# Kernel tuning notes

Hardware: AMD Instinct MI355X
Metric: run time of the kernel (lower is better)

Reference implementation:

```python
import jax, jax.numpy as jnp
import numpy as np

B, C, H, W = 1, 512, 64, 64
HEADS, DH = 8, 64
DI = HEADS * DH          # 512 = heads * dim_head
SW = 8                   # sliding window size
CB = 16                  # compress block size
SB = 2                   # selection block size
NSEL = 2                 # num selected blocks
N = H * W                # 4096 tokens
NCB = N // CB            # 256 compress blocks
NFB = N // SB            # 2048 fine (selection) blocks
NEG = jnp.finfo(jnp.float32).min


def setup_inputs() -> dict:
    key = jax.random.key(0)
    ks = jax.random.split(key, 24)
    rn = lambda k, shape, s=0.03: jax.random.normal(k, shape, jnp.float32) * s
    return dict(
        x=jax.random.normal(ks[0], (B, C, H, W), jnp.float32),
        w_in=rn(ks[1], (C, C)), b_in=jnp.zeros((C,), jnp.float32),
        g_norm=jnp.ones((C,), jnp.float32),
        wq=rn(ks[2], (DI, C)), wk=rn(ks[3], (DI, C)), wv=rn(ks[4], (DI, C)),
        k_pos=rn(ks[5], (HEADS, CB, DH), 0.02), v_pos=rn(ks[6], (HEADS, CB, DH), 0.02),
        mem_k=rn(ks[7], (HEADS, 1, DH), 0.02), mem_v=rn(ks[8], (HEADS, 1, DH), 0.02),
        kc_w1=rn(ks[9], (CB * DH, CB * DH)), kc_b1=jnp.zeros((CB * DH,), jnp.float32),
        kc_w2=rn(ks[10], (DH, CB * DH)), kc_b2=jnp.zeros((DH,), jnp.float32),
        vc_w1=rn(ks[11], (CB * DH, CB * DH)), vc_b1=jnp.zeros((CB * DH,), jnp.float32),
        vc_w2=rn(ks[12], (DH, CB * DH)), vc_b2=jnp.zeros((DH,), jnp.float32),
        w_strat=rn(ks[13], (3 * HEADS, C)), b_strat=jnp.zeros((3 * HEADS,), jnp.float32),
        w_comb=rn(ks[14], (C, DI)),
        w_out=rn(ks[15], (C, C)), b_out=jnp.zeros((C,), jnp.float32),
    )


def _rope(x):
    # rotary-embedding-torch default: theta=10000, interleaved pairs
    d = x.shape[-1]
    inv = 1.0 / (10000.0 ** (jnp.arange(0, d, 2, dtype=jnp.float32) / d))
    ang = jnp.arange(x.shape[-2], dtype=jnp.float32)[:, None] * inv  # (n, d/2)
    cos = jnp.repeat(jnp.cos(ang), 2, axis=-1)
    sin = jnp.repeat(jnp.sin(ang), 2, axis=-1)
    xp = x.reshape(x.shape[:-1] + (d // 2, 2))
    xr = jnp.stack((-xp[..., 1], xp[..., 0]), axis=-1).reshape(x.shape)
    return x * cos + xr * sin


def reference(x, w_in, b_in, g_norm, wq, wk, wv, k_pos, v_pos, mem_k, mem_v,
              kc_w1, kc_b1, kc_w2, kc_b2, vc_w1, vc_b1, vc_w2, vc_b2,
              w_strat, b_strat, w_comb, w_out, b_out):
    scale = DH ** -0.5
    # proj_in (1x1 conv) then flatten to sequence (b, n, c); residual uses this
    xs = jnp.einsum('bchw,oc->bohw', x, w_in) + b_in[None, :, None, None]
    seq = xs.reshape(B, C, N).transpose(0, 2, 1)
    # RMSNorm
    h = seq * jax.lax.rsqrt(jnp.mean(seq * seq, -1, keepdims=True) + 1e-6) * g_norm
    # qkv -> (b, heads, n, d)
    q = (h @ wq.T).reshape(B, N, HEADS, DH).transpose(0, 2, 1, 3)
    k = (h @ wk.T).reshape(B, N, HEADS, DH).transpose(0, 2, 1, 3)
    v = (h @ wv.T).reshape(B, N, HEADS, DH).transpose(0, 2, 1, 3)

    # ---- 1. compressed attention (block compression MLP + mem kv) ----
    kin = (k + jnp.tile(k_pos, (1, NCB, 1))[None]).reshape(B, HEADS, NCB, CB * DH)
    vin = (v + jnp.tile(v_pos, (1, NCB, 1))[None]).reshape(B, HEADS, NCB, CB * DH)
    ck = jax.nn.relu(kin @ kc_w1.T + kc_b1) @ kc_w2.T + kc_b2   # (b,h,NCB,d)
    cv = jax.nn.relu(vin @ vc_w1.T + vc_b1) @ vc_w2.T + vc_b2
    ck = jnp.concatenate([jnp.broadcast_to(mem_k[None], (B, HEADS, 1, DH)), ck], axis=2)
    cv = jnp.concatenate([jnp.broadcast_to(mem_v[None], (B, HEADS, 1, DH)), cv], axis=2)
    ck_seq = jnp.concatenate([jnp.array([-1]), (jnp.arange(NCB) + 1) * CB - 1])
    cmask = ck_seq[None, :] < jnp.arange(N)[:, None]             # (N, NCB+1), True=attend
    csim = jnp.einsum('bhid,bhjd->bhij', q, ck) * scale
    csim = jnp.where(cmask[None, None], csim, NEG)
    compressed_out = jnp.einsum('bhij,bhjd->bhid', jax.nn.softmax(csim, axis=-1), cv)

    # rotary positions for fine + sliding branches
    rq, rk = _rope(q), _rope(k)

    # ---- 2. fine selection attention ----
    # importance at fine-block granularity; since SB divides CB, each fine block
    # maps to exactly one compress block (equivalent to repeat->mask->mean in torch)
    imp = csim[..., 1:]                                          # drop mem kv logits
    fb_of = jnp.arange(NFB) // (CB // SB)
    imp_fine = imp[..., fb_of]                                   # (b,h,N,NFB)
    blk_causal = jnp.arange(NFB)[None, :] < (jnp.arange(N) // SB)[:, None]
    imp_fine = jnp.where(blk_causal[None, None], imp_fine, -jnp.inf)
    logits = jnp.concatenate([jnp.full((B, HEADS, N, 1), -1e3, jnp.float32), imp_fine], axis=-1)
    probs = jax.nn.softmax(logits, axis=-1)[..., 1:]             # (b,h,N,NFB)
    sel_val, sel_idx = jax.lax.top_k(probs, NSEL)                # (b,h,N,NSEL)
    diag_idx = jnp.broadcast_to((jnp.arange(N) // SB)[None, None, :, None], (B, HEADS, N, 1))
    sel_idx = jnp.concatenate([sel_idx, diag_idx], axis=-1)      # append own (diagonal) block
    fmask_sel = jnp.repeat((sel_val > 1e-10)[..., None], SB, axis=-1)   # (b,h,N,NSEL,SB)
    diag_mask = jnp.arange(SB)[None, :] <= (jnp.arange(N) % SB)[:, None]  # within-block causal
    diag_mask = jnp.broadcast_to(diag_mask[None, None, :, None, :], (B, HEADS, N, 1, SB))
    fmask = jnp.concatenate([fmask_sel, diag_mask], axis=-2).reshape(B, HEADS, N, (NSEL + 1) * SB)
    fk_blk = rk.reshape(B, HEADS, NFB, SB, DH)
    fv_blk = v.reshape(B, HEADS, NFB, SB, DH)
    idx = sel_idx.reshape(B, HEADS, N * (NSEL + 1))[..., None, None]
    fk = jnp.take_along_axis(fk_blk, idx, axis=2).reshape(B, HEADS, N, (NSEL + 1) * SB, DH)
    fv = jnp.take_along_axis(fv_blk, idx, axis=2).reshape(B, HEADS, N, (NSEL + 1) * SB, DH)
    fsim = jnp.einsum('bhid,bhijd->bhij', rq, fk) * scale
    fsim = jnp.where(fmask, fsim, NEG)
    fine_out = jnp.einsum('bhij,bhijd->bhid', jax.nn.softmax(fsim, axis=-1), fv)

    # ---- 3. sliding window attention (causal, exact window: 0 <= i-j <= SW) ----
    kp = jnp.pad(rk, ((0, 0), (0, 0), (SW, 0), (0, 0)))
    vp = jnp.pad(v, ((0, 0), (0, 0), (SW, 0), (0, 0)))
    widx = jnp.arange(N)[:, None] + jnp.arange(SW + 1)[None, :]  # indices into padded seq
    kw = kp[:, :, widx]                                          # (b,h,N,SW+1,d)
    vw = vp[:, :, widx]
    wvalid = (jnp.arange(N)[:, None] - SW + jnp.arange(SW + 1)[None, :]) >= 0
    ssim = jnp.einsum('bhid,bhijd->bhij', rq, kw) * scale
    ssim = jnp.where(wvalid[None, None], ssim, NEG)
    slide_out = jnp.einsum('bhij,bhijd->bhid', jax.nn.softmax(ssim, axis=-1), vw)

    # ---- combine the three strategies with learned sigmoid gates ----
    gates = jax.nn.sigmoid(h @ w_strat.T + b_strat).reshape(B, N, HEADS, 3).transpose(0, 2, 1, 3)
    out = gates[..., 0:1] * compressed_out + gates[..., 1:2] * fine_out + gates[..., 2:3] * slide_out
    out = out.transpose(0, 2, 1, 3).reshape(B, N, DI) @ w_comb.T  # merge heads + combine
    out2d = out.transpose(0, 2, 1).reshape(B, C, H, W)
    return jnp.einsum('bchw,oc->bohw', out2d, w_out) + b_out[None, :, None, None] + xs
```

## Files before the change

### kernel.cpp

```cpp
#include <hip/hip_runtime.h>
#include <hip/hip_bf16.h>
#include <math.h>

typedef __attribute__((ext_vector_type(8))) short s8v;
typedef __attribute__((ext_vector_type(8))) _Float16 h8v;
typedef __attribute__((ext_vector_type(4))) float f4v;
typedef __hip_bfloat16 bf16;

#define NEGF (-3.40282346638528859812e+38f)
#define QSMEM 20480

enum { EPI_F32 = 0, EPI_BIAS, EPI_BRELU_BF16, EPI_BF16, EPI_FINAL };

__device__ __forceinline__ float wred_sum(float v) {
#pragma unroll
  for (int m = 1; m < 64; m <<= 1) v += __shfl_xor(v, m, 64);
  return v;
}

template <int EPI>
__device__ __forceinline__ void bgemm_body(char* smem, int bx, int by, int bz,
    const bf16* __restrict__ A, const bf16* __restrict__ B, void* __restrict__ C,
    int K, int ldC, long sA, long sB, long sC,
    const float* __restrict__ bias, const void* __restrict__ aux) {
  short (*Ahs)[2048] = (short(*)[2048])smem;
  short (*Bhs)[2048] = (short(*)[2048])(smem + 2 * 2048 * 2);
  const short* ah = (const short*)A + (long)bz * sA;
  const short* bh = (const short*)B + (long)bz * sB;
  int tid = threadIdx.x;
  int wv_ = tid >> 6, lane = tid & 63;
  int lrow = tid >> 2, lcol = (tid & 3) << 3;
  int lidx = lrow * 32 + lcol;
  long abase = (long)(bx * 64 + lrow) * K + lcol;
  long bbase = (long)(by * 64 + lrow) * K + lcol;
  int frow = lane & 15, fk = (lane >> 4) << 3;
  int aoff = (wv_ * 16 + frow) * 32 + fk;
  f4v acc[4] = {};
  {
    s8v avh = *(const s8v*)&ah[abase];
    s8v bvh = *(const s8v*)&bh[bbase];
    *(s8v*)&Ahs[0][lidx] = avh;
    *(s8v*)&Bhs[0][lidx] = bvh;
  }
  __syncthreads();
  int nit = K >> 5, buf = 0;
  for (int it = 0; it < nit; it++) {
    s8v avh, bvh;
    bool pf = (it + 1 < nit);
    if (pf) {
      long ko = (long)(it + 1) << 5;
      avh = *(const s8v*)&ah[abase + ko];
      bvh = *(const s8v*)&bh[bbase + ko];
    }
    s8v afh = *(const s8v*)&Ahs[buf][aoff];
#pragma unroll
    for (int nt = 0; nt < 4; nt++) {
      s8v bfh = *(const s8v*)&Bhs[buf][(nt * 16 + frow) * 32 + fk];
      acc[nt] = __builtin_amdgcn_mfma_f32_16x16x32_bf16(afh, bfh, acc[nt], 0, 0, 0);
    }
    if (pf) {
      *(s8v*)&Ahs[buf ^ 1][lidx] = avh;
      *(s8v*)&Bhs[buf ^ 1][lidx] = bvh;
      __syncthreads();
      buf ^= 1;
    }
  }
  int rb = bx * 64 + wv_ * 16 + ((lane >> 4) << 2);
#pragma unroll
  for (int nt = 0; nt < 4; nt++) {
    int gn = by * 64 + nt * 16 + (lane & 15);
#pragma unroll
    for (int rg = 0; rg < 4; rg++) {
      int gm = rb + rg;
      float v = acc[nt][rg];
      long ci = (long)bz * sC + (long)gm * ldC + gn;
      if (EPI == EPI_F32) ((float*)C)[ci] = v;
      else if (EPI == EPI_BIAS) ((float*)C)[ci] = v + bias[gn];
      else if (EPI == EPI_BRELU_BF16) ((bf16*)C)[ci] = __float2bfloat16(fmaxf(v + bias[gn], 0.f));
      else if (EPI == EPI_BF16) ((bf16*)C)[ci] = __float2bfloat16(v);
      else if (EPI == EPI_FINAL)
        ((float*)C)[ci] = v + bias[gm] + ((const float*)aux)[(long)gn * 512 + gm];
    }
  }
}


#define HX_DECL                                                     \
  short* L = (short*)smem;                                          \
  const int MS = 64 * 40;                                           \
  int tid = threadIdx.x;                                            \
  int wv = tid >> 6, lane = tid & 63;                               \
  int lrow = tid >> 2, lcol = (tid & 3) << 3;                       \
  int frow = lane & 15, fk = (lane >> 4) << 3;                      \
  int aoff = (wv * 16 + frow) * 40 + fk;                            \
  int soff = lrow * 40 + lcol;                                      \
  f4v acc0[4] = {}, accx[4] = {}, acc2[4] = {};

#define HX_STAGE0                                                   \
  {                                                                 \
    *(h8v*)&L[0 * MS + soff] = *(const h8v*)&Ah[abase];             \
    *(h8v*)&L[1 * MS + soff] = *(const h8v*)&Al[abase];             \
    *(h8v*)&L[2 * MS + soff] = *(const h8v*)&Bh[bbase];             \
    *(h8v*)&L[3 * MS + soff] = *(const h8v*)&Bl[bbase];             \
  }                                                                 \
  __syncthreads();

#define HX_LOOP(NIT)                                                \
  for (int it = 0; it < (NIT); it++) {                              \
    h8v pah, pal, pbh, pbl;                                         \
    bool pf = (it + 1 < (NIT));                                     \
    if (pf) {                                                       \
      long ko = (long)(it + 1) << 5;                                \
      pah = *(const h8v*)&Ah[abase + ko];                           \
      pal = *(const h8v*)&Al[abase + ko];                           \
      pbh = *(const h8v*)&Bh[bbase + ko];                           \
      pbl = *(const h8v*)&Bl[bbase + ko];                           \
    }                                                               \
    h8v ah = *(const h8v*)&L[aoff];                                 \
    h8v al = *(const h8v*)&L[MS + aoff];                            \
    _Pragma("unroll") for (int nt = 0; nt < 4; nt++) {              \
      int bo = 2 * MS + (nt * 16 + frow) * 40 + fk;                 \
      h8v bh = *(const h8v*)&L[bo];                                 \
      h8v bl = *(const h8v*)&L[bo + MS];                            \
      acc0[nt] = __builtin_amdgcn_mfma_f32_16x16x32_f16(ah, bh, acc0[nt], 0, 0, 0); \
      accx[nt] = __builtin_amdgcn_mfma_f32_16x16x32_f16(ah, bl, accx[nt], 0, 0, 0); \
      accx[nt] = __builtin_amdgcn_mfma_f32_16x16x32_f16(al, bh, accx[nt], 0, 0, 0); \
      acc2[nt] = __builtin_amdgcn_mfma_f32_16x16x32_f16(al, bl, acc2[nt], 0, 0, 0); \
    }                                                               \
    if (pf) {                                                       \
      __syncthreads();                                              \
      *(h8v*)&L[soff] = pah;                                        \
      *(h8v*)&L[MS + soff] = pal;                                   \
      *(h8v*)&L[2 * MS + soff] = pbh;                               \
      *(h8v*)&L[3 * MS + soff] = pbl;                               \
      __syncthreads();                                              \
    }                                                               \
  }

#define HX_COMBINE(nt, rg) \
  (acc0[nt][rg] + (accx[nt][rg] + acc2[nt][rg] * (1.f / 4096.f)) * (1.f / 4096.f))

__device__ __forceinline__ void qk_f16_body(char* smem, int bx, int by,
    const _Float16* __restrict__ Ah, const _Float16* __restrict__ Al,
    const _Float16* __restrict__ Bh, const _Float16* __restrict__ Bl,
    _Float16* __restrict__ qhh, _Float16* __restrict__ qhl,
    _Float16* __restrict__ kinh, _Float16* __restrict__ kinl,
    float* __restrict__ rq, float* __restrict__ rk, const float* __restrict__ kpos) {
  HX_DECL
  long abase = (long)(bx * 64 + lrow) * 512 + lcol;
  long bbase = (long)(by * 64 + lrow) * 512 + lcol;
  HX_STAGE0
  HX_LOOP(16)
  bool isq = by < 8;
  int h = by & 7;
  int rb = wv * 16 + ((lane >> 4) << 2);
#pragma unroll
  for (int nt = 0; nt < 4; nt++) {
    int dloc = nt * 16 + frow;
    int d2 = dloc >> 1;
    float inv = exp2f((float)d2 * -0.4152410118609203f);
#pragma unroll
    for (int rg = 0; rg < 4; rg++) {
      int n = bx * 64 + rb + rg;
      float vf = HX_COMBINE(nt, rg);
      float ang = (float)n * inv;
      float sv, cv;
      sincosf(ang, &sv, &cv);
      float vp = __shfl_xor(vf, 1, 64);
      float rr = (dloc & 1) ? (vf * cv + vp * sv) : (vf * cv - vp * sv);
      long oi = ((long)h * 4096 + n) * 64 + dloc;
      if (isq) {
        _Float16 hi = (_Float16)vf;
        qhh[oi] = hi;
        qhl[oi] = (_Float16)((vf - (float)hi) * 4096.f);
        rq[oi] = rr;
      } else {
        rk[oi] = rr;
        float kv = vf + kpos[(h * 16 + (n & 15)) * 64 + dloc];
        _Float16 khi = (_Float16)kv;
        long ki = (((long)h * 256 + (n >> 4)) * 16 + (n & 15)) * 64 + dloc;
        kinh[ki] = khi;
        kinl[ki] = (_Float16)((kv - (float)khi) * 4096.f);
      }
    }
  }
}

__device__ __forceinline__ void hx_conv_body(char* smem, int bx, int by,
    const _Float16* __restrict__ Ah, const _Float16* __restrict__ Al,
    const _Float16* __restrict__ Bh, const _Float16* __restrict__ Bl,
    float* __restrict__ C, const float* __restrict__ bias) {
  HX_DECL
  long abase = (long)(bx * 64 + lrow) * 512 + lcol;
  long bbase = (long)(by * 64 + lrow) * 512 + lcol;
  HX_STAGE0
  HX_LOOP(16)
  int rb = bx * 64 + wv * 16 + ((lane >> 4) << 2);
#pragma unroll
  for (int nt = 0; nt < 4; nt++) {
    int gn = by * 64 + nt * 16 + frow;
#pragma unroll
    for (int rg = 0; rg < 4; rg++) {
      int gm = rb + rg;
      C[(long)gm * 512 + gn] = HX_COMBINE(nt, rg) + bias[gn];
    }
  }
}

__device__ __forceinline__ void hx_mlp1_body(char* smem, int bx, int by,
    const _Float16* __restrict__ Ah, const _Float16* __restrict__ Al,
    const _Float16* __restrict__ Bh, const _Float16* __restrict__ Bl,
    _Float16* __restrict__ Ch, _Float16* __restrict__ Cl, const float* __restrict__ bias) {
  HX_DECL
  long abase = (long)(bx * 64 + lrow) * 1024 + lcol;
  long bbase = (long)(by * 64 + lrow) * 1024 + lcol;
  HX_STAGE0
  HX_LOOP(32)
  int rb = bx * 64 + wv * 16 + ((lane >> 4) << 2);
#pragma unroll
  for (int nt = 0; nt < 4; nt++) {
    int gn = by * 64 + nt * 16 + frow;
#pragma unroll
    for (int rg = 0; rg < 4; rg++) {
      int gm = rb + rg;
      float v = fmaxf(HX_COMBINE(nt, rg) + bias[gn], 0.f);
      _Float16 hi = (_Float16)v;
      long ci = (long)gm * 1024 + gn;
      Ch[ci] = hi;
      Cl[ci] = (_Float16)((v - (float)hi) * 4096.f);
    }
  }
}

__device__ __forceinline__ void hx_ksplit_body(char* smem, int bx, int by,
    const _Float16* __restrict__ Ah, const _Float16* __restrict__ Al,
    const _Float16* __restrict__ Bh, const _Float16* __restrict__ Bl,
    float* __restrict__ P) {
  HX_DECL
  long kbeg = (long)by << 7;
  long abase = (long)(bx * 64 + lrow) * 1024 + kbeg + lcol;
  long bbase = (long)lrow * 1024 + kbeg + lcol;
  HX_STAGE0
  HX_LOOP(4)
  float* p = P + (long)by * 131072;
  int rb = bx * 64 + wv * 16 + ((lane >> 4) << 2);
#pragma unroll
  for (int nt = 0; nt < 4; nt++) {
    int gn = nt * 16 + frow;
#pragma unroll
    for (int rg = 0; rg < 4; rg++) {
      int gm = rb + rg;
      p[(long)gm * 64 + gn] = HX_COMBINE(nt, rg);
    }
  }
}

__device__ __forceinline__ void hx_csim_body(char* smem, int bx, int by, int bz,
    const _Float16* __restrict__ Ah, const _Float16* __restrict__ Al,
    const _Float16* __restrict__ Bh, const _Float16* __restrict__ Bl,
    float* __restrict__ C) {
  HX_DECL
  long abase = ((long)bz * 4096 + bx * 64 + lrow) * 64 + lcol;
  long bbase = ((long)bz * 320 + by * 64 + lrow) * 64 + lcol;
  HX_STAGE0
  HX_LOOP(2)
  int rb = bx * 64 + wv * 16 + ((lane >> 4) << 2);
#pragma unroll
  for (int nt = 0; nt < 4; nt++) {
    int gn = by * 64 + nt * 16 + frow;
#pragma unroll
    for (int rg = 0; rg < 4; rg++) {
      int gm = rb + rg;
      C[((long)bz * 4096 + gm) * 320 + gn] = HX_COMBINE(nt, rg) * 0.125f;
    }
  }
}

__device__ __forceinline__ void prep_elem(long i,
    const float* __restrict__ wq, const float* __restrict__ wk, const float* __restrict__ wv,
    const float* __restrict__ wst, const float* __restrict__ bst,
    const float* __restrict__ kc_w1, const float* __restrict__ kc_w2,
    const float* __restrict__ vc_w1, const float* __restrict__ vc_w2, const float* __restrict__ w_comb,
    const float* __restrict__ w_out, _Float16* __restrict__ wqkh, _Float16* __restrict__ wqkl,
    bf16* __restrict__ wvs, float* __restrict__ bias2,
    _Float16* __restrict__ kw1h, _Float16* __restrict__ kw1l,
    _Float16* __restrict__ kw2h, _Float16* __restrict__ kw2l, bf16* __restrict__ vw1b,
    bf16* __restrict__ vw2b, bf16* __restrict__ wcombb, bf16* __restrict__ woutb) {
  if (i < 524288) {
    int r = (int)(i >> 9), c = (int)(i & 511);
    float w = (r < 512) ? wq[i] : wk[(r - 512) * 512 + c];
    _Float16 hi = (_Float16)w;
    wqkh[i] = hi;
    wqkl[i] = (_Float16)((w - (float)hi) * 4096.f);
    return;
  }
  i -= 524288;
  if (i < 294912) {
    int r = (int)(i >> 9), c = (int)(i & 511);
    float v = 0.f;
    if (r < 512) v = wv[i];
    else if (r < 536) v = wst[(r - 512) * 512 + c];
    wvs[i] = __float2bfloat16(v);
    if (i < 576) bias2[i] = (i >= 512 && i < 536) ? bst[i - 512] : 0.f;
    return;
  }
  i -= 294912;
  if (i < 1048576) {
    float w = kc_w1[i];
    _Float16 hi = (_Float16)w;
    kw1h[i] = hi;
    kw1l[i] = (_Float16)((w - (float)hi) * 4096.f);
    return;
  }
  i -= 1048576;
  if (i < 65536) {
    float w = kc_w2[i];
    _Float16 hi = (_Float16)w;
    kw2h[i] = hi;
    kw2l[i] = (_Float16)((w - (float)hi) * 4096.f);
    return;
  }
  i -= 65536;
  if (i < 1048576) { vw1b[i] = __float2bfloat16(vc_w1[i]); return; }
  i -= 1048576;
  if (i < 65536) { vw2b[i] = __float2bfloat16(vc_w2[i]); return; }
  i -= 65536;
  if (i < 262144) { wcombb[i] = __float2bfloat16(w_comb[i]); return; }
  i -= 262144;
  if (i < 262144) woutb[i] = __float2bfloat16(w_out[i]);
}
#define PREP_TOTAL 3571712l

template <int EPI>
__global__ __launch_bounds__(256) void gemm_bt(
    const bf16* __restrict__ A, const bf16* __restrict__ B, void* __restrict__ C,
    int K, int ldC, long sA, long sB, long sC,
    const float* __restrict__ bias, const void* __restrict__ aux) {
  __shared__ char smem[4 * 2048 * 2];
  bgemm_body<EPI>(smem, blockIdx.x, blockIdx.y, blockIdx.z, A, B, C, K, ldC, sA, sB, sC, bias, aux);
}

__global__ __launch_bounds__(256) void k_conv_prep(
    const _Float16* __restrict__ xth, const _Float16* __restrict__ xtl,
    const _Float16* __restrict__ winh, const _Float16* __restrict__ winl,
    float* __restrict__ xsf, const float* __restrict__ b_in,
    const float* __restrict__ wq, const float* __restrict__ wk, const float* __restrict__ wv,
    const float* __restrict__ wst, const float* __restrict__ bst,
    const float* __restrict__ kc_w1, const float* __restrict__ kc_w2,
    const float* __restrict__ vc_w1, const float* __restrict__ vc_w2, const float* __restrict__ w_comb,
    const float* __restrict__ w_out, _Float16* __restrict__ wqkh, _Float16* __restrict__ wqkl,
    bf16* __restrict__ wvs, float* __restrict__ bias2,
    _Float16* __restrict__ kw1h, _Float16* __restrict__ kw1l,
    _Float16* __restrict__ kw2h, _Float16* __restrict__ kw2l, bf16* __restrict__ vw1b,
    bf16* __restrict__ vw2b, bf16* __restrict__ wcombb, bf16* __restrict__ woutb) {
  __shared__ char smem[QSMEM];
  if (blockIdx.y < 8) {
    hx_conv_body(smem, blockIdx.x, blockIdx.y, xth, xtl, winh, winl, xsf, b_in);
  } else {
    long base = (((long)(blockIdx.y - 8) * 64 + blockIdx.x) * 256) + threadIdx.x;
    for (long i = base; i < PREP_TOTAL; i += 16l * 64 * 256)
      prep_elem(i, wq, wk, wv, wst, bst, kc_w1, kc_w2, vc_w1, vc_w2, w_comb, w_out,
                wqkh, wqkl, wvs, bias2, kw1h, kw1l, kw2h, kw2l, vw1b, vw2b, wcombb, woutb);
  }
}

__global__ __launch_bounds__(256) void k_fused_qk_t2(
    const _Float16* __restrict__ hhi, const _Float16* __restrict__ hlo,
    const _Float16* __restrict__ wqkh, const _Float16* __restrict__ wqkl,
    _Float16* __restrict__ qhh, _Float16* __restrict__ qhl,
    _Float16* __restrict__ kinh, _Float16* __restrict__ kinl,
    float* __restrict__ rq, float* __restrict__ rk, const float* __restrict__ kpos,
    const bf16* __restrict__ hbf, const bf16* __restrict__ wvs, float* __restrict__ T2,
    const float* __restrict__ bias2) {
  __shared__ char smem[QSMEM];
  if (blockIdx.y >= 16) {
    bgemm_body<EPI_BIAS>(smem, blockIdx.x, blockIdx.y - 16, 0, hbf, wvs, T2, 512, 576, 0, 0, 0, bias2,
                         nullptr);
    return;
  }
  qk_f16_body(smem, blockIdx.x, blockIdx.y, hhi, hlo, wqkh, wqkl, qhh, qhl, kinh, kinl, rq, rk, kpos);
}

__global__ void k_repackV(const float* __restrict__ T2, const float* __restrict__ vpos,
                          float* __restrict__ vvv, bf16* __restrict__ vin) {
  int e = blockIdx.x * 256 + threadIdx.x;
  int d = e & 63, n = (e >> 6) & 4095, h = e >> 18;
  float v0 = T2[(long)n * 576 + h * 64 + d];
  vvv[((long)h * 4096 + n) * 64 + d] = v0;
  vin[(((long)h * 256 + (n >> 4)) * 16 + (n & 15)) * 64 + d] =
      __float2bfloat16(v0 + vpos[(h * 16 + (n & 15)) * 64 + d]);
}

__global__ __launch_bounds__(256) void k_fused_mlp1(
    const _Float16* __restrict__ kinh, const _Float16* __restrict__ kinl,
    const _Float16* __restrict__ kw1h, const _Float16* __restrict__ kw1l,
    _Float16* __restrict__ hidh, _Float16* __restrict__ hidl, const float* __restrict__ kb1,
    const bf16* __restrict__ vin, const bf16* __restrict__ vw1,
    bf16* __restrict__ hidv, const float* __restrict__ vb1) {
  __shared__ char smem[QSMEM];
  if (blockIdx.y < 16)
    hx_mlp1_body(smem, blockIdx.x, blockIdx.y, kinh, kinl, kw1h, kw1l, hidh, hidl, kb1);
  else
    bgemm_body<EPI_BRELU_BF16>(smem, blockIdx.x, blockIdx.y - 16, 0, vin, vw1, hidv, 1024, 1024, 0, 0, 0,
                               vb1, nullptr);
}

__global__ __launch_bounds__(256) void k_fused_mlp2(
    const _Float16* __restrict__ hidh, const _Float16* __restrict__ hidl,
    const _Float16* __restrict__ kw2h, const _Float16* __restrict__ kw2l, float* __restrict__ kpart,
    const bf16* __restrict__ hidv, const bf16* __restrict__ vw2, float* __restrict__ cvc,
    const float* __restrict__ vb2) {
  __shared__ char smem[QSMEM];
  if (blockIdx.y < 8)
    hx_ksplit_body(smem, blockIdx.x, blockIdx.y, hidh, hidl, kw2h, kw2l, kpart);
  else
    bgemm_body<EPI_BIAS>(smem, blockIdx.x, 0, 0, hidv, vw2, cvc, 1024, 64, 0, 0, 0, vb2, nullptr);
}

__global__ __launch_bounds__(256) void k_csim(
    const _Float16* __restrict__ qhh, const _Float16* __restrict__ qhl,
    const _Float16* __restrict__ ckbh, const _Float16* __restrict__ ckbl, float* __restrict__ csim) {
  __shared__ char smem[QSMEM];
  hx_csim_body(smem, blockIdx.x, blockIdx.y, blockIdx.z, qhh, qhl, ckbh, ckbl, csim);
}

__global__ void k_transpose16(const float* __restrict__ x, _Float16* __restrict__ xth,
                              _Float16* __restrict__ xtl,
                              const float* __restrict__ w_in, _Float16* __restrict__ winh,
                              _Float16* __restrict__ winl) {
  if (blockIdx.y == 16) {
    int tid = threadIdx.y * 32 + threadIdx.x;
    long base = (long)blockIdx.x * 256 + tid;
    for (long i = base; i < 262144; i += 128l * 256) {
      float w = w_in[i];
      _Float16 hi = (_Float16)w;
      winh[i] = hi;
      winl[i] = (_Float16)((w - (float)hi) * 4096.f);
    }
    return;
  }
  __shared__ float t[32][33];
  int n0 = blockIdx.x * 32, c0 = blockIdx.y * 32;
  int tx = threadIdx.x, ty = threadIdx.y;
#pragma unroll
  for (int r = ty; r < 32; r += 8) t[r][tx] = x[(long)(c0 + r) * 4096 + n0 + tx];
  __syncthreads();
#pragma unroll
  for (int r = ty; r < 32; r += 8) {
    float v = t[tx][r];
    _Float16 hi = (_Float16)v;
    long o = (long)(n0 + r) * 512 + c0 + tx;
    xth[o] = hi;
    xtl[o] = (_Float16)((v - (float)hi) * 4096.f);
  }
}

__global__ __launch_bounds__(256) void k_rmsnorm(const float* __restrict__ xs, const float* __restrict__ g,
                                                 _Float16* __restrict__ hhi, _Float16* __restrict__ hlo,
                                                 bf16* __restrict__ hbf) {
  int n = blockIdx.x, t = threadIdx.x;
  const float* row = xs + (long)n * 512;
  double a = (double)row[t], b = (double)row[t + 256];
  double ss = a * a + b * b;
#pragma unroll
  for (int m = 1; m < 64; m <<= 1) ss += __shfl_xor(ss, m, 64);
  __shared__ double red[4];
  if ((t & 63) == 0) red[t >> 6] = ss;
  __syncthreads();
  double tot = red[0] + red[1] + red[2] + red[3];
  double r = 1.0 / sqrt(tot / 512.0 + 1e-6);
  double h0 = a * r * (double)g[t], h1 = b * r * (double)g[t + 256];
  long o = (long)n * 512 + t;
  float f0 = (float)h0, f1 = (float)h1;
  _Float16 a0 = (_Float16)f0, a1 = (_Float16)f1;
  hhi[o] = a0;
  hhi[o + 256] = a1;
  hlo[o] = (_Float16)((f0 - (float)a0) * 4096.f);
  hlo[o + 256] = (_Float16)((f1 - (float)a1) * 4096.f);
  hbf[o] = __float2bfloat16(f0);
  hbf[o + 256] = __float2bfloat16(f1);
}

__global__ void k_repackB(const float* __restrict__ kpart, const float* __restrict__ cvc,
                          const float* __restrict__ mem_k, const float* __restrict__ mem_v,
                          const float* __restrict__ kb2, _Float16* __restrict__ ckbh,
                          _Float16* __restrict__ ckbl, bf16* __restrict__ cvtb) {
  int g = blockIdx.x * 256 + threadIdx.x;
  if (g < 8 * 320 * 64) {
    int d = g & 63, j = (g >> 6) % 320, h = g / (320 * 64);
    float vf = 0.f;
    if (j == 0) vf = mem_k[h * 64 + d];
    else if (j < 257) {
      long ri = ((long)h * 256 + (j - 1)) * 64 + d;
      double s = 0.0;
#pragma unroll
      for (int p = 0; p < 8; p++) s += (double)kpart[(long)p * 131072 + ri];
      vf = (float)(s + (double)kb2[d]);
    }
    _Float16 hi = (_Float16)vf;
    ckbh[g] = hi;
    ckbl[g] = (_Float16)((vf - (float)hi) * 4096.f);
  }
  if (g < 8 * 64 * 288) {
    int j = g % 288, d = (g / 288) & 63, h = g / (288 * 64);
    float v = 0.f;
    if (j == 0) v = mem_v[h * 64 + d];
    else if (j < 257) v = cvc[((long)h * 256 + (j - 1)) * 64 + d];
    cvtb[g] = __float2bfloat16(v);
  }
}

__global__ __launch_bounds__(256) void k_selsm(const float* __restrict__ csim, bf16* __restrict__ pb,
                                               int4* __restrict__ selb) {
  int r = blockIdx.x * 4 + (threadIdx.x >> 6);
  int lane = threadIdx.x & 63;
  int i = r & 4095;
  const float* row = csim + (long)r * 320;
  int nv = i / 16 + 1;
  float s[5], e[5];
  float mx = -INFINITY;
#pragma unroll
  for (int t = 0; t < 5; t++) {
    int j = lane + 64 * t;
    float v = (j < nv) ? row[j] : -INFINITY;
    s[t] = v;
    mx = fmaxf(mx, v);
  }
#pragma unroll
  for (int m = 1; m < 64; m <<= 1) mx = fmaxf(mx, __shfl_xor(mx, m, 64));
  float sum = 0.f;
#pragma unroll
  for (int t = 0; t < 5; t++) {
    int j = lane + 64 * t;
    e[t] = (j < nv) ? __expf(s[t] - mx) : 0.f;
    sum += e[t];
  }
  sum = wred_sum(sum);
  float rinv = 1.f / sum;
  bf16* prow = pb + (long)r * 288;
#pragma unroll
  for (int t = 0; t < 5; t++) {
    int j = lane + 64 * t;
    if (j < 288) prow[j] = __float2bfloat16((j < nv) ? e[t] * rinv : 0.f);
  }
  int nvb = i >> 1;
  int nmv = (nvb + 7) >> 3;
  float vm[4];
  float bestv = -INFINITY;
  int bestm = 0x7fffffff;
#pragma unroll
  for (int t = 0; t < 4; t++) {
    int m = lane + 64 * t;
    float v = -INFINITY;
    if (m < nmv) v = (m + 1 < nv) ? row[m + 1] : NEGF;
    vm[t] = v;
    if (v > bestv) { bestv = v; bestm = m; }
  }
#pragma unroll
  for (int mk = 1; mk < 64; mk <<= 1) {
    float ov = __shfl_xor(bestv, mk, 64);
    int om = __shfl_xor(bestm, mk, 64);
    if (ov > bestv || (ov == bestv && om < bestm)) { bestv = ov; bestm = om; }
  }
  int m0 = bestm;
  int cnt0 = min(8, nvb - 8 * m0);
  float rv = -INFINITY;
  int rm = 0x7fffffff;
#pragma unroll
  for (int t = 0; t < 4; t++) {
    int m = lane + 64 * t;
    if (m != m0 && vm[t] > rv) { rv = vm[t]; rm = m; }
  }
#pragma unroll
  for (int mk = 1; mk < 64; mk <<= 1) {
    float ov = __shfl_xor(rv, mk, 64);
    int om = __shfl_xor(rm, mk, 64);
    if (ov > rv || (ov == rv && om < rm)) { rv = ov; rm = om; }
  }
  float Ml = fmaxf(-1000.f, bestv);
  float z = 0.f;
#pragma unroll
  for (int t = 0; t < 4; t++) {
    int m = lane + 64 * t;
    if (m < nmv) z += (float)min(8, nvb - 8 * m) * expf(vm[t] - Ml);
  }
  z = wred_sum(z) + expf(-1000.f - Ml);
  int fb0 = 0, fb1 = 0, mk0 = 0, mk1 = 0;
  if (nmv > 0) {
    float sv0 = expf(bestv - Ml) / z;
    fb0 = 8 * m0;
    mk0 = sv0 > 1e-10f;
    if (cnt0 >= 2) { fb1 = fb0 + 1; mk1 = mk0; }
    else if (nmv > 1) {
      float sv1 = expf(rv - Ml) / z;
      fb1 = 8 * rm;
      mk1 = sv1 > 1e-10f;
    }
  }
  if (lane == 0) selb[r] = make_int4(fb0, fb1, mk0, mk1);
}

__global__ __launch_bounds__(256) void k_fineslide(const float* __restrict__ rq, const float* __restrict__ rk,
                                                   const float* __restrict__ vv, const float* __restrict__ co,
                                                   const int4* __restrict__ selb, const float* __restrict__ T2,
                                                   bf16* __restrict__ comb) {
  int r = blockIdx.x * 4 + (threadIdx.x >> 6);
  int d = threadIdx.x & 63;
  int h = r >> 12, i = r & 4095;
  long hb = (long)h * 4096 * 64;
  float qd = rq[hb + (long)i * 64 + d];
  int4 s4 = selb[r];
  int dg = i >> 1;
  int tok[6] = {2 * s4.x, 2 * s4.x + 1, 2 * s4.y, 2 * s4.y + 1, 2 * dg, 2 * dg + 1};
  int ok6[6] = {s4.z, s4.z, s4.w, s4.w, 1, (i & 1)};
  float sim[6], val[6];
#pragma unroll
  for (int j = 0; j < 6; j++) {
    float kd = rk[hb + (long)tok[j] * 64 + d];
    val[j] = vv[hb + (long)tok[j] * 64 + d];
    float p = wred_sum(qd * kd);
    sim[j] = ok6[j] ? p * 0.125f : NEGF;
  }
  float mx = sim[0];
#pragma unroll
  for (int j = 1; j < 6; j++) mx = fmaxf(mx, sim[j]);
  float den = 0.f, fo = 0.f;
#pragma unroll
  for (int j = 0; j < 6; j++) {
    float e_ = __expf(sim[j] - mx);
    den += e_;
    fo += e_ * val[j];
  }
  fo /= den;
  float ssim[9], sval[9];
#pragma unroll
  for (int t = 0; t < 9; t++) {
    int tk = i - 8 + t;
    int okt = tk >= 0;
    int tc = okt ? tk : 0;
    float kd = rk[hb + (long)tc * 64 + d];
    sval[t] = okt ? vv[hb + (long)tc * 64 + d] : 0.f;
    float p = wred_sum(qd * kd);
    ssim[t] = okt ? p * 0.125f : NEGF;
  }
  float mx2 = ssim[8];
#pragma unroll
  for (int t = 0; t < 8; t++) mx2 = fmaxf(mx2, ssim[t]);
  float den2 = 0.f, so = 0.f;
#pragma unroll
  for (int t = 0; t < 9; t++) {
    float e_ = __expf(ssim[t] - mx2);
    den2 += e_;
    so += e_ * sval[t];
  }
  so /= den2;
  const float* gb = T2 + (long)i * 576 + 512 + h * 3;
  float g0 = 1.f / (1.f + __expf(-gb[0]));
  float g1 = 1.f / (1.f + __expf(-gb[1]));
  float g2 = 1.f / (1.f + __expf(-gb[2]));
  float cd = co[hb + (long)i * 64 + d];
  comb[(long)i * 512 + h * 64 + d] = __float2bfloat16(g0 * cd + g1 * fo + g2 * so);
}

extern "C" void kernel_launch(void* const* d_in, const int* in_sizes, int n_in, void* d_out, int out_size,
                              void* d_ws, size_t ws_size, hipStream_t stream) {
  (void)in_sizes; (void)n_in; (void)out_size; (void)ws_size;
  const float* x = (const float*)d_in[0];
  const float* w_in = (const float*)d_in[1];
  const float* b_in = (const float*)d_in[2];
  const float* g_norm = (const float*)d_in[3];
  const float* wq = (const float*)d_in[4];
  const float* wk = (const float*)d_in[5];
  const float* wv = (const float*)d_in[6];
  const float* k_pos = (const float*)d_in[7];
  const float* v_pos = (const float*)d_in[8];
  const float* mem_k = (const float*)d_in[9];
  const float* mem_v = (const float*)d_in[10];
  const float* kc_w1 = (const float*)d_in[11];
  const float* kc_b1 = (const float*)d_in[12];
  const float* kc_w2 = (const float*)d_in[13];
  const float* kc_b2 = (const float*)d_in[14];
  const float* vc_w1 = (const float*)d_in[15];
  const float* vc_b1 = (const float*)d_in[16];
  const float* vc_w2 = (const float*)d_in[17];
  const float* vc_b2 = (const float*)d_in[18];
  const float* w_strat = (const float*)d_in[19];
  const float* b_strat = (const float*)d_in[20];
  const float* w_comb = (const float*)d_in[21];
  const float* w_out = (const float*)d_in[22];
  const float* b_out = (const float*)d_in[23];

  char* wsp = (char*)d_ws;
  size_t off = 0;
  auto alloc = [&](size_t b) -> void* {
    void* p = wsp + off;
    off += (b + 255) & ~(size_t)255;
    return p;
  };
  float* xsf = (float*)alloc(4096l * 512 * 4);
  _Float16* hhi = (_Float16*)alloc(4096l * 512 * 2);
  _Float16* hlo = (_Float16*)alloc(4096l * 512 * 2);
  bf16* hbf = (bf16*)alloc(4096l * 512 * 2);
  _Float16* winh = (_Float16*)alloc(512l * 512 * 2);
  _Float16* winl = (_Float16*)alloc(512l * 512 * 2);
  _Float16* wqkh = (_Float16*)alloc(1024l * 512 * 2);
  _Float16* wqkl = (_Float16*)alloc(1024l * 512 * 2);
  bf16* wvs = (bf16*)alloc(576l * 512 * 2);
  float* bias2 = (float*)alloc(576 * 4);
  float* T2 = (float*)alloc(4096l * 576 * 4);
  float* csim = (float*)alloc(8l * 4096 * 320 * 4);
  _Float16* qhh = (_Float16*)alloc(8l * 4096 * 64 * 2);
  _Float16* qhl = (_Float16*)alloc(8l * 4096 * 64 * 2);
  float* rq = (float*)alloc(8l * 4096 * 64 * 4);
  float* rk = (float*)alloc(8l * 4096 * 64 * 4);
  float* vvb = (float*)alloc(8l * 4096 * 64 * 4);
  char* xthl = (char*)alloc(2l * 4096 * 512 * 2);
  _Float16* xth = (_Float16*)xthl;
  _Float16* xtl = xth + 4096l * 512;
  _Float16* hidh = xth;
  _Float16* hidl = xtl;
  char* kinpb = (char*)alloc(2048l * 1024 * 8 + 2048l * 1024 * 2);
  _Float16* kinh = (_Float16*)kinpb;
  _Float16* kinl = kinh + 2048l * 1024;
  bf16* vinb = (bf16*)(kinpb + 2l * 2048 * 1024 * 2);
  bf16* pb = (bf16*)kinpb;
  _Float16* kw1h = (_Float16*)alloc(1024l * 1024 * 2);
  _Float16* kw1l = (_Float16*)alloc(1024l * 1024 * 2);
  _Float16* kw2h = (_Float16*)alloc(64l * 1024 * 2);
  _Float16* kw2l = (_Float16*)alloc(64l * 1024 * 2);
  bf16* vw1b = (bf16*)alloc(1024l * 1024 * 2);
  bf16* vw2b = (bf16*)alloc(64l * 1024 * 2);
  bf16* hidv = (bf16*)alloc(2048l * 1024 * 2);
  float* cvc = (float*)alloc(2048l * 64 * 4);
  _Float16* ckbh = (_Float16*)alloc(8l * 320 * 64 * 2);
  _Float16* ckbl = (_Float16*)alloc(8l * 320 * 64 * 2);
  bf16* cvtb = (bf16*)alloc(8l * 64 * 288 * 2);
  int4* selb = (int4*)alloc(32768l * 16);
  float* co = (float*)alloc(8l * 4096 * 64 * 4);
  bf16* comb = (bf16*)alloc(4096l * 512 * 2);
  bf16* zb = (bf16*)alloc(4096l * 512 * 2);
  bf16* wcombb = (bf16*)alloc(512l * 512 * 2);
  bf16* woutb = (bf16*)alloc(512l * 512 * 2);
  float* kpart = (float*)alloc(8l * 2048 * 64 * 4);

  k_transpose16<<<dim3(128, 17), dim3(32, 8), 0, stream>>>(x, xth, xtl, w_in, winh, winl);
  k_conv_prep<<<dim3(64, 24), 256, 0, stream>>>(xth, xtl, winh, winl, xsf, b_in, wq, wk, wv, w_strat,
                                                b_strat, kc_w1, kc_w2, vc_w1, vc_w2, w_comb, w_out,
                                                wqkh, wqkl, wvs, bias2, kw1h, kw1l, kw2h, kw2l,
                                                vw1b, vw2b, wcombb, woutb);
  k_rmsnorm<<<4096, 256, 0, stream>>>(xsf, g_norm, hhi, hlo, hbf);
  k_fused_qk_t2<<<dim3(64, 25, 1), 256, 0, stream>>>(hhi, hlo, wqkh, wqkl, qhh, qhl, kinh, kinl, rq, rk,
                                                     k_pos, hbf, wvs, T2, bias2);
  k_repackV<<<8192, 256, 0, stream>>>(T2, v_pos, vvb, vinb);
  k_fused_mlp1<<<dim3(32, 32, 1), 256, 0, stream>>>(kinh, kinl, kw1h, kw1l, hidh, hidl, kc_b1, vinb, vw1b,
                                                    hidv, vc_b1);
  k_fused_mlp2<<<dim3(32, 9, 1), 256, 0, stream>>>(hidh, hidl, kw2h, kw2l, kpart, hidv, vw2b, cvc, vc_b2);
  k_repackB<<<640, 256, 0, stream>>>(kpart, cvc, mem_k, mem_v, kc_b2, ckbh, ckbl, cvtb);
  k_csim<<<dim3(64, 5, 8), 256, 0, stream>>>(qhh, qhl, ckbh, ckbl, csim);
  k_selsm<<<8192, 256, 0, stream>>>(csim, pb, selb);
  gemm_bt<EPI_F32><<<dim3(64, 1, 8), 256, 0, stream>>>(pb, cvtb, co, 288, 64, 4096l * 288, 64l * 288,
                                                       4096l * 64, nullptr, nullptr);
  k_fineslide<<<8192, 256, 0, stream>>>(rq, rk, vvb, co, selb, T2, comb);
  gemm_bt<EPI_BF16><<<dim3(64, 8, 1), 256, 0, stream>>>(comb, wcombb, zb, 512, 512, 0, 0, 0, nullptr, nullptr);
  gemm_bt<EPI_FINAL><<<dim3(8, 64, 1), 256, 0, stream>>>(woutb, zb, d_out, 512, 4096, 0, 0, 0, b_out, xsf);
}
```

Baseline: 331.5 us.

## Pad GEMM LDS, double-register prefetch, precompute rope table, skip masked csim tiles

Pads the bf16 GEMM shared-memory row stride to 40 to reduce LDS bank conflicts. Both the bf16 and split-f16 GEMM loops are unrolled by two with two register sets, so global loads for tile k+2 are issued while tile k is computed. Rope sin/cos values are computed once into a table in the transpose kernel instead of calling sincosf in the QK epilogue. The compressed-similarity kernel early-exits for tiles that are entirely causally masked, which relies on downstream code never reading those unwritten entries.

```diff
diff --git a/kernel.cpp b/kernel.cpp
--- a/kernel.cpp
+++ b/kernel.cpp
@@ -9,6 +9,7 @@
 
 #define NEGF (-3.40282346638528859812e+38f)
 #define QSMEM 20480
+#define BSMEM 20480
 
 enum { EPI_F32 = 0, EPI_BIAS, EPI_BRELU_BF16, EPI_BF16, EPI_FINAL };
 
@@ -23,18 +24,18 @@
     const bf16* __restrict__ A, const bf16* __restrict__ B, void* __restrict__ C,
     int K, int ldC, long sA, long sB, long sC,
     const float* __restrict__ bias, const void* __restrict__ aux) {
-  short (*Ahs)[2048] = (short(*)[2048])smem;
-  short (*Bhs)[2048] = (short(*)[2048])(smem + 2 * 2048 * 2);
+  short (*Ahs)[2560] = (short(*)[2560])smem;
+  short (*Bhs)[2560] = (short(*)[2560])(smem + 2 * 2560 * 2);
   const short* ah = (const short*)A + (long)bz * sA;
   const short* bh = (const short*)B + (long)bz * sB;
   int tid = threadIdx.x;
   int wv_ = tid >> 6, lane = tid & 63;
   int lrow = tid >> 2, lcol = (tid & 3) << 3;
-  int lidx = lrow * 32 + lcol;
+  int lidx = lrow * 40 + lcol;
   long abase = (long)(bx * 64 + lrow) * K + lcol;
   long bbase = (long)(by * 64 + lrow) * K + lcol;
   int frow = lane & 15, fk = (lane >> 4) << 3;
-  int aoff = (wv_ * 16 + frow) * 32 + fk;
+  int aoff = (wv_ * 16 + frow) * 40 + fk;
   f4v acc[4] = {};
   {
     s8v avh = *(const s8v*)&ah[abase];
@@ -44,27 +45,46 @@
   }
   __syncthreads();
   int nit = K >> 5, buf = 0;
-  for (int it = 0; it < nit; it++) {
-    s8v avh, bvh;
-    bool pf = (it + 1 < nit);
-    if (pf) {
-      long ko = (long)(it + 1) << 5;
-      avh = *(const s8v*)&ah[abase + ko];
-      bvh = *(const s8v*)&bh[bbase + ko];
-    }
-    s8v afh = *(const s8v*)&Ahs[buf][aoff];
-#pragma unroll
-    for (int nt = 0; nt < 4; nt++) {
-      s8v bfh = *(const s8v*)&Bhs[buf][(nt * 16 + frow) * 32 + fk];
-      acc[nt] = __builtin_amdgcn_mfma_f32_16x16x32_bf16(afh, bfh, acc[nt], 0, 0, 0);
-    }
-    if (pf) {
-      *(s8v*)&Ahs[buf ^ 1][lidx] = avh;
-      *(s8v*)&Bhs[buf ^ 1][lidx] = bvh;
+  s8v rAa, rAb, rBa, rBb;
+  if (nit > 1) {
+    rAa = *(const s8v*)&ah[abase + 32];
+    rAb = *(const s8v*)&bh[bbase + 32];
+  }
+#define B_DSMFMA                                                       \
+  {                                                                    \
+    s8v afh = *(const s8v*)&Ahs[buf][aoff];                            \
+    _Pragma("unroll") for (int nt = 0; nt < 4; nt++) {                 \
+      s8v bfh = *(const s8v*)&Bhs[buf][(nt * 16 + frow) * 40 + fk];    \
+      acc[nt] = __builtin_amdgcn_mfma_f32_16x16x32_bf16(afh, bfh, acc[nt], 0, 0, 0); \
+    }                                                                  \
+  }
+  for (int it = 0; it < nit; it += 2) {
+    if (it + 2 < nit) {
+      long ko = (long)(it + 2) << 5;
+      rBa = *(const s8v*)&ah[abase + ko];
+      rBb = *(const s8v*)&bh[bbase + ko];
+    }
+    B_DSMFMA
+    if (it + 1 < nit) {
+      *(s8v*)&Ahs[buf ^ 1][lidx] = rAa;
+      *(s8v*)&Bhs[buf ^ 1][lidx] = rAb;
       __syncthreads();
       buf ^= 1;
-    }
-  }
+      if (it + 3 < nit) {
+        long ko = (long)(it + 3) << 5;
+        rAa = *(const s8v*)&ah[abase + ko];
+        rAb = *(const s8v*)&bh[bbase + ko];
+      }
+      B_DSMFMA
+      if (it + 2 < nit) {
+        *(s8v*)&Ahs[buf ^ 1][lidx] = rBa;
+        *(s8v*)&Bhs[buf ^ 1][lidx] = rBb;
+        __syncthreads();
+        buf ^= 1;
+      }
+    }
+  }
+#undef B_DSMFMA
   int rb = bx * 64 + wv_ * 16 + ((lane >> 4) << 2);
 #pragma unroll
   for (int nt = 0; nt < 4; nt++) {
@@ -105,17 +125,8 @@
   }                                                                 \
   __syncthreads();
 
-#define HX_LOOP(NIT)                                                \
-  for (int it = 0; it < (NIT); it++) {                              \
-    h8v pah, pal, pbh, pbl;                                         \
-    bool pf = (it + 1 < (NIT));                                     \
-    if (pf) {                                                       \
-      long ko = (long)(it + 1) << 5;                                \
-      pah = *(const h8v*)&Ah[abase + ko];                           \
-      pal = *(const h8v*)&Al[abase + ko];                           \
-      pbh = *(const h8v*)&Bh[bbase + ko];                           \
-      pbl = *(const h8v*)&Bl[bbase + ko];                           \
-    }                                                               \
+#define HX_DSMFMA                                                   \
+  {                                                                 \
     h8v ah = *(const h8v*)&L[aoff];                                 \
     h8v al = *(const h8v*)&L[MS + aoff];                            \
     _Pragma("unroll") for (int nt = 0; nt < 4; nt++) {              \
@@ -127,13 +138,48 @@
       accx[nt] = __builtin_amdgcn_mfma_f32_16x16x32_f16(al, bh, accx[nt], 0, 0, 0); \
       acc2[nt] = __builtin_amdgcn_mfma_f32_16x16x32_f16(al, bl, acc2[nt], 0, 0, 0); \
     }                                                               \
-    if (pf) {                                                       \
+  }
+
+#define HX_LOOP(NIT)                                                \
+  h8v rAa, rAb, rAc, rAd, rBa, rBb, rBc, rBd;                       \
+  if ((NIT) > 1) {                                                  \
+    rAa = *(const h8v*)&Ah[abase + 32];                             \
+    rAb = *(const h8v*)&Al[abase + 32];                             \
+    rAc = *(const h8v*)&Bh[bbase + 32];                             \
+    rAd = *(const h8v*)&Bl[bbase + 32];                             \
+  }                                                                 \
+  for (int it = 0; it < (NIT); it += 2) {                           \
+    if (it + 2 < (NIT)) {                                           \
+      long ko = (long)(it + 2) << 5;                                \
+      rBa = *(const h8v*)&Ah[abase + ko];                           \
+      rBb = *(const h8v*)&Al[abase + ko];                           \
+      rBc = *(const h8v*)&Bh[bbase + ko];                           \
+      rBd = *(const h8v*)&Bl[bbase + ko];                           \
+    }                                                               \
+    HX_DSMFMA                                                       \
+    if (it + 1 < (NIT)) {                                           \
       __syncthreads();                                              \
-      *(h8v*)&L[soff] = pah;                                        \
-      *(h8v*)&L[MS + soff] = pal;                                   \
-      *(h8v*)&L[2 * MS + soff] = pbh;                               \
-      *(h8v*)&L[3 * MS + soff] = pbl;                               \
+      *(h8v*)&L[soff] = rAa;                                        \
+      *(h8v*)&L[MS + soff] = rAb;                                   \
+      *(h8v*)&L[2 * MS + soff] = rAc;                               \
+      *(h8v*)&L[3 * MS + soff] = rAd;                               \
       __syncthreads();                                              \
+      if (it + 3 < (NIT)) {                                         \
+        long ko = (long)(it + 3) << 5;                              \
+        rAa = *(const h8v*)&Ah[abase + ko];                         \
+        rAb = *(const h8v*)&Al[abase + ko];                         \
+        rAc = *(const h8v*)&Bh[bbase + ko];                         \
+        rAd = *(const h8v*)&Bl[bbase + ko];                         \
+      }                                                             \
+      HX_DSMFMA                                                     \
+      if (it + 2 < (NIT)) {                                         \
+        __syncthreads();                                            \
+        *(h8v*)&L[soff] = rBa;                                      \
+        *(h8v*)&L[MS + soff] = rBb;                                 \
+        *(h8v*)&L[2 * MS + soff] = rBc;                             \
+        *(h8v*)&L[3 * MS + soff] = rBd;                             \
+        __syncthreads();                                            \
+      }                                                             \
     }                                                               \
   }
 
@@ -145,7 +191,8 @@
     const _Float16* __restrict__ Bh, const _Float16* __restrict__ Bl,
     _Float16* __restrict__ qhh, _Float16* __restrict__ qhl,
     _Float16* __restrict__ kinh, _Float16* __restrict__ kinl,
-    float* __restrict__ rq, float* __restrict__ rk, const float* __restrict__ kpos) {
+    float* __restrict__ rq, float* __restrict__ rk, const float* __restrict__ kpos,
+    const float2* __restrict__ ropet) {
   HX_DECL
   long abase = (long)(bx * 64 + lrow) * 512 + lcol;
   long bbase = (long)(by * 64 + lrow) * 512 + lcol;
@@ -158,14 +205,12 @@
   for (int nt = 0; nt < 4; nt++) {
     int dloc = nt * 16 + frow;
     int d2 = dloc >> 1;
-    float inv = exp2f((float)d2 * -0.4152410118609203f);
 #pragma unroll
     for (int rg = 0; rg < 4; rg++) {
       int n = bx * 64 + rb + rg;
       float vf = HX_COMBINE(nt, rg);
-      float ang = (float)n * inv;
-      float sv, cv;
-      sincosf(ang, &sv, &cv);
+      float2 cs = ropet[(long)n * 32 + d2];
+      float sv = cs.x, cv = cs.y;
       float vp = __shfl_xor(vf, 1, 64);
       float rr = (dloc & 1) ? (vf * cv + vp * sv) : (vf * cv - vp * sv);
       long oi = ((long)h * 4096 + n) * 64 + dloc;
@@ -336,7 +381,7 @@
     const bf16* __restrict__ A, const bf16* __restrict__ B, void* __restrict__ C,
     int K, int ldC, long sA, long sB, long sC,
     const float* __restrict__ bias, const void* __restrict__ aux) {
-  __shared__ char smem[4 * 2048 * 2];
+  __shared__ char smem[BSMEM];
   bgemm_body<EPI>(smem, blockIdx.x, blockIdx.y, blockIdx.z, A, B, C, K, ldC, sA, sB, sC, bias, aux);
 }
 
@@ -370,6 +415,7 @@
     _Float16* __restrict__ qhh, _Float16* __restrict__ qhl,
     _Float16* __restrict__ kinh, _Float16* __restrict__ kinl,
     float* __restrict__ rq, float* __restrict__ rk, const float* __restrict__ kpos,
+    const float2* __restrict__ ropet,
     const bf16* __restrict__ hbf, const bf16* __restrict__ wvs, float* __restrict__ T2,
     const float* __restrict__ bias2) {
   __shared__ char smem[QSMEM];
@@ -378,7 +424,8 @@
                          nullptr);
     return;
   }
-  qk_f16_body(smem, blockIdx.x, blockIdx.y, hhi, hlo, wqkh, wqkl, qhh, qhl, kinh, kinl, rq, rk, kpos);
+  qk_f16_body(smem, blockIdx.x, blockIdx.y, hhi, hlo, wqkh, wqkl, qhh, qhl, kinh, kinl, rq, rk, kpos,
+              ropet);
 }
 
 __global__ void k_repackV(const float* __restrict__ T2, const float* __restrict__ vpos,
@@ -420,6 +467,7 @@
 __global__ __launch_bounds__(256) void k_csim(
     const _Float16* __restrict__ qhh, const _Float16* __restrict__ qhl,
     const _Float16* __restrict__ ckbh, const _Float16* __restrict__ ckbl, float* __restrict__ csim) {
+  if (blockIdx.y * 64 > blockIdx.x * 4 + 3) return;
   __shared__ char smem[QSMEM];
   hx_csim_body(smem, blockIdx.x, blockIdx.y, blockIdx.z, qhh, qhl, ckbh, ckbl, csim);
 }
@@ -427,15 +475,24 @@
 __global__ void k_transpose16(const float* __restrict__ x, _Float16* __restrict__ xth,
                               _Float16* __restrict__ xtl,
                               const float* __restrict__ w_in, _Float16* __restrict__ winh,
-                              _Float16* __restrict__ winl) {
+                              _Float16* __restrict__ winl, float2* __restrict__ ropet) {
   if (blockIdx.y == 16) {
     int tid = threadIdx.y * 32 + threadIdx.x;
     long base = (long)blockIdx.x * 256 + tid;
-    for (long i = base; i < 262144; i += 128l * 256) {
-      float w = w_in[i];
-      _Float16 hi = (_Float16)w;
-      winh[i] = hi;
-      winl[i] = (_Float16)((w - (float)hi) * 4096.f);
+    for (long i = base; i < 393216; i += 128l * 256) {
+      if (i < 262144) {
+        float w = w_in[i];
+        _Float16 hi = (_Float16)w;
+        winh[i] = hi;
+        winl[i] = (_Float16)((w - (float)hi) * 4096.f);
+      } else {
+        int idx = (int)(i - 262144);
+        int d2 = idx & 31, n = idx >> 5;
+        float inv = exp2f((float)d2 * -0.4152410118609203f);
+        float sv, cv;
+        sincosf((float)n * inv, &sv, &cv);
+        ropet[idx] = make_float2(sv, cv);
+      }
     }
     return;
   }
@@ -707,6 +764,7 @@
   _Float16* wqkl = (_Float16*)alloc(1024l * 512 * 2);
   bf16* wvs = (bf16*)alloc(576l * 512 * 2);
   float* bias2 = (float*)alloc(576 * 4);
+  float2* ropet = (float2*)alloc(4096l * 32 * 8);
   float* T2 = (float*)alloc(4096l * 576 * 4);
   float* csim = (float*)alloc(8l * 4096 * 320 * 4);
   _Float16* qhh = (_Float16*)alloc(8l * 4096 * 64 * 2);
@@ -743,14 +801,14 @@
   bf16* woutb = (bf16*)alloc(512l * 512 * 2);
   float* kpart = (float*)alloc(8l * 2048 * 64 * 4);
 
-  k_transpose16<<<dim3(128, 17), dim3(32, 8), 0, stream>>>(x, xth, xtl, w_in, winh, winl);
+  k_transpose16<<<dim3(128, 17), dim3(32, 8), 0, stream>>>(x, xth, xtl, w_in, winh, winl, ropet);
   k_conv_prep<<<dim3(64, 24), 256, 0, stream>>>(xth, xtl, winh, winl, xsf, b_in, wq, wk, wv, w_strat,
                                                 b_strat, kc_w1, kc_w2, vc_w1, vc_w2, w_comb, w_out,
                                                 wqkh, wqkl, wvs, bias2, kw1h, kw1l, kw2h, kw2l,
                                                 vw1b, vw2b, wcombb, woutb);
   k_rmsnorm<<<4096, 256, 0, stream>>>(xsf, g_norm, hhi, hlo, hbf);
   k_fused_qk_t2<<<dim3(64, 25, 1), 256, 0, stream>>>(hhi, hlo, wqkh, wqkl, qhh, qhl, kinh, kinl, rq, rk,
-                                                     k_pos, hbf, wvs, T2, bias2);
+                                                     k_pos, ropet, hbf, wvs, T2, bias2);
   k_repackV<<<8192, 256, 0, stream>>>(T2, v_pos, vvb, vinb);
   k_fused_mlp1<<<dim3(32, 32, 1), 256, 0, stream>>>(kinh, kinl, kw1h, kw1l, hidh, hidl, kc_b1, vinb, vw1b,
                                                     hidv, vc_b1);
```

After: 325.6 us. About the same (-1.8%).
